# Optimization experiments

Hardware: AMD Instinct MI355X
Metric: run time of the kernel (lower is better)

The kernel has to match this reference:

```python
import jax, jax.numpy as jnp
import numpy as np

N0, N1, N2 = 360448, 22528, 2048
E0, E1 = 337920, 20480
D = 256


def setup_inputs() -> dict:
    key = jax.random.key(0)
    ks = jax.random.split(key, 12)
    s = 1.0 / np.sqrt(D)
    return {
        "x": jax.random.normal(ks[0], (N0, D), dtype=jnp.float32),
        "src0": jax.random.randint(ks[1], (E0,), 0, N0, dtype=jnp.int32),
        "dst0": jax.random.randint(ks[2], (E0,), 0, N1, dtype=jnp.int32),
        "src1": jax.random.randint(ks[3], (E1,), 0, N1, dtype=jnp.int32),
        "dst1": jax.random.randint(ks[4], (E1,), 0, N2, dtype=jnp.int32),
        "Wl0": jax.random.normal(ks[5], (D, D), dtype=jnp.float32) * s,
        "bl0": jnp.zeros((D,), dtype=jnp.float32),
        "Wr0": jax.random.normal(ks[6], (D, D), dtype=jnp.float32) * s,
        "Wl1": jax.random.normal(ks[7], (D, D), dtype=jnp.float32) * s,
        "bl1": jnp.zeros((D,), dtype=jnp.float32),
        "Wr1": jax.random.normal(ks[8], (D, D), dtype=jnp.float32) * s,
    }


def _sage_conv(x_src, x_tgt, src, dst, n_tgt, Wl, bl, Wr):
    # mean aggregation of source neighbor features per target node
    summed = jax.ops.segment_sum(x_src[src], dst, num_segments=n_tgt)
    cnt = jax.ops.segment_sum(jnp.ones((src.shape[0],), x_src.dtype), dst,
                              num_segments=n_tgt)
    agg = summed / jnp.maximum(cnt, 1.0)[:, None]
    # PyG SAGEConv: lin_l(agg) + lin_r(x_target); lin_r has no bias
    return agg @ Wl.T + bl + x_tgt @ Wr.T


def reference(x, src0, dst0, src1, dst1, Wl0, bl0, Wr0, Wl1, bl1, Wr1):
    # layer 0: [N0, D] -> [N1, D]
    h = _sage_conv(x, x[:N1], src0, dst0, N1, Wl0, bl0, Wr0)
    h = jax.nn.relu(h)  # dropout is identity in eval mode
    # layer 1: [N1, D] -> [N2, D]
    out = _sage_conv(h, h[:N2], src1, dst1, N2, Wl1, bl1, Wr1)
    return out
```

## Files before the change

kernel.cpp:

```cpp
#include <hip/hip_runtime.h>
#include <hip/hip_bf16.h>

#define N0C 360448
#define N1C 22528
#define N2C 2048

typedef __attribute__((ext_vector_type(8))) short bf16x8;
typedef __attribute__((ext_vector_type(4))) float f32x4;
typedef __attribute__((ext_vector_type(2))) int i32x2;

__device__ __forceinline__ short f2bf(float f) {
    union { float f; unsigned u; } x; x.f = f;
    unsigned r = x.u + 0x7fff + ((x.u >> 16) & 1);
    return (short)(r >> 16);
}
__device__ __forceinline__ float bf2f(unsigned short u) {
    union { unsigned u; float f; } x; x.u = ((unsigned)u) << 16;
    return x.f;
}

__global__ __launch_bounds__(256)
void prep_kernel(const float* __restrict__ Wl0, const float* __restrict__ Wr0,
                 const float* __restrict__ Wl1, const float* __restrict__ Wr1,
                 short* __restrict__ Wcat0, short* __restrict__ Wcat1,
                 int* __restrict__ hist0, int* __restrict__ hist1) {
    const int stride = gridDim.x * blockDim.x;
    const int t0 = blockIdx.x * blockDim.x + threadIdx.x;
    for (int i = t0; i < 2 * 256 * 512; i += stride) {
        int layer = i >> 17;
        int r = i & ((1 << 17) - 1);
        int j = r >> 9, k = r & 511;
        const float* Wl = layer ? Wl1 : Wl0;
        const float* Wr = layer ? Wr1 : Wr0;
        float v = (k < 256) ? Wl[j * 256 + k] : Wr[j * 256 + (k - 256)];
        (layer ? Wcat1 : Wcat0)[r] = f2bf(v);
    }
    for (int i = t0; i < N1C + N2C; i += stride) {
        if (i < N1C) hist0[i] = 0; else hist1[i - N1C] = 0;
    }
}

__global__ void hist_both_kernel(const int* __restrict__ dst0, int E0,
                                 const int* __restrict__ dst1, int E1,
                                 int* __restrict__ hist0, int* __restrict__ hist1) {
    const int stride = gridDim.x * blockDim.x;
    for (int i = blockIdx.x * blockDim.x + threadIdx.x; i < E0 + E1; i += stride) {
        if (i < E0) atomicAdd(&hist0[dst0[i]], 1);
        else        atomicAdd(&hist1[dst1[i - E0]], 1);
    }
}

__global__ __launch_bounds__(1024)
void scan_both_kernel(const int* __restrict__ hist0, int* __restrict__ rowptr0,
                      int* __restrict__ cursor0,
                      const int* __restrict__ hist1, int* __restrict__ rowptr1,
                      int* __restrict__ cursor1) {
    __shared__ int wsum[16];
    const int N = (blockIdx.x == 0) ? N1C : N2C;
    const int* hist   = (blockIdx.x == 0) ? hist0 : hist1;
    int* rowptr       = (blockIdx.x == 0) ? rowptr0 : rowptr1;
    int* cursor       = (blockIdx.x == 0) ? cursor0 : cursor1;
    const int tid = threadIdx.x;
    const int lane = tid & 63;
    const int wid = tid >> 6;
    const int per = (N + 1023) >> 10;
    const int start = min(tid * per, N);
    const int end = min(start + per, N);
    int s = 0;
    for (int i = start; i < end; ++i) s += hist[i];
    int incl = s;
#pragma unroll
    for (int d = 1; d < 64; d <<= 1) {
        int t = __shfl_up(incl, d);
        if (lane >= d) incl += t;
    }
    if (lane == 63) wsum[wid] = incl;
    __syncthreads();
    if (wid == 0) {
        int v = (lane < 16) ? wsum[lane] : 0;
#pragma unroll
        for (int d = 1; d < 16; d <<= 1) {
            int t = __shfl_up(v, d);
            if (lane >= d) v += t;
        }
        if (lane < 16) wsum[lane] = v;
    }
    __syncthreads();
    int off = (wid > 0 ? wsum[wid - 1] : 0) + (incl - s);
    for (int i = start; i < end; ++i) {
        rowptr[i] = off;
        cursor[i] = off;
        off += hist[i];
    }
    if (tid == 1023) rowptr[N] = wsum[15];
}

__global__ void fill_both_kernel(const int* __restrict__ src0, const int* __restrict__ dst0, int E0,
                                 const int* __restrict__ src1, const int* __restrict__ dst1, int E1,
                                 int* __restrict__ cursor0, int* __restrict__ eidx0,
                                 int* __restrict__ cursor1, int* __restrict__ eidx1) {
    const int stride = gridDim.x * blockDim.x;
    for (int i = blockIdx.x * blockDim.x + threadIdx.x; i < E0 + E1; i += stride) {
        if (i < E0) {
            int p = atomicAdd(&cursor0[dst0[i]], 1);
            eidx0[p] = src0[i];
        } else {
            int p = atomicAdd(&cursor1[dst1[i - E0]], 1);
            eidx1[p] = src1[i - E0];
        }
    }
}

__global__ __launch_bounds__(256)
void gather0_kernel(const float* __restrict__ x, const int* __restrict__ rowptr,
                    const int* __restrict__ eidx, short* __restrict__ Acat0) {
    const int wv = (blockIdx.x * 256 + threadIdx.x) >> 6;
    const int lane = threadIdx.x & 63;
    if (wv >= N1C) return;
    const int co = lane * 4;

    const float4 xr = *(const float4*)(x + (size_t)wv * 256 + co);

    const int beg = rowptr[wv];
    const int end = rowptr[wv + 1];
    f32x4 acc = {0.f, 0.f, 0.f, 0.f};
    f32x4 acc2 = {0.f, 0.f, 0.f, 0.f};
    int j = beg;
    for (; j + 7 < end; j += 8) {
        const f32x4 v0 = *(const f32x4*)(x + (size_t)eidx[j    ] * 256 + co);
        const f32x4 v1 = *(const f32x4*)(x + (size_t)eidx[j + 1] * 256 + co);
        const f32x4 v2 = *(const f32x4*)(x + (size_t)eidx[j + 2] * 256 + co);
        const f32x4 v3 = *(const f32x4*)(x + (size_t)eidx[j + 3] * 256 + co);
        const f32x4 v4 = *(const f32x4*)(x + (size_t)eidx[j + 4] * 256 + co);
        const f32x4 v5 = *(const f32x4*)(x + (size_t)eidx[j + 5] * 256 + co);
        const f32x4 v6 = *(const f32x4*)(x + (size_t)eidx[j + 6] * 256 + co);
        const f32x4 v7 = *(const f32x4*)(x + (size_t)eidx[j + 7] * 256 + co);
        acc  += v0 + v1 + v2 + v3;
        acc2 += v4 + v5 + v6 + v7;
    }
    for (; j + 1 < end; j += 2) {
        const f32x4 v0 = *(const f32x4*)(x + (size_t)eidx[j    ] * 256 + co);
        const f32x4 v1 = *(const f32x4*)(x + (size_t)eidx[j + 1] * 256 + co);
        acc += v0 + v1;
    }
    if (j < end)
        acc2 += *(const f32x4*)(x + (size_t)eidx[j] * 256 + co);
    acc += acc2;

    const float sc = 1.0f / fmaxf((float)(end - beg), 1.0f);
    union { short s[4]; i32x2 i; } o;
    o.s[0] = f2bf(acc.x * sc); o.s[1] = f2bf(acc.y * sc);
    o.s[2] = f2bf(acc.z * sc); o.s[3] = f2bf(acc.w * sc);
    __builtin_nontemporal_store(o.i, (i32x2*)(Acat0 + (size_t)wv * 512 + co));

    union { short s[4]; i32x2 i; } xo;
    xo.s[0] = f2bf(xr.x); xo.s[1] = f2bf(xr.y);
    xo.s[2] = f2bf(xr.z); xo.s[3] = f2bf(xr.w);
    __builtin_nontemporal_store(xo.i, (i32x2*)(Acat0 + (size_t)wv * 512 + 256 + co));
}

__global__ __launch_bounds__(256)
void gather1_kernel(const ushort* __restrict__ X, const int* __restrict__ rowptr,
                    const int* __restrict__ eidx, short* __restrict__ Acat, int N) {
    const int wv = (blockIdx.x * 256 + threadIdx.x) >> 6;
    const int lane = threadIdx.x & 63;
    if (wv >= N) return;
    const int beg = rowptr[wv];
    const int end = rowptr[wv + 1];
    float a0 = 0.f, a1 = 0.f, a2 = 0.f, a3 = 0.f;
    int j = beg;
    for (; j + 1 < end; j += 2) {
        int s0 = eidx[j], s1 = eidx[j + 1];
        ushort4 v0 = *(const ushort4*)(X + (size_t)s0 * 256 + lane * 4);
        ushort4 v1 = *(const ushort4*)(X + (size_t)s1 * 256 + lane * 4);
        a0 += bf2f(v0.x) + bf2f(v1.x); a1 += bf2f(v0.y) + bf2f(v1.y);
        a2 += bf2f(v0.z) + bf2f(v1.z); a3 += bf2f(v0.w) + bf2f(v1.w);
    }
    if (j < end) {
        ushort4 v0 = *(const ushort4*)(X + (size_t)eidx[j] * 256 + lane * 4);
        a0 += bf2f(v0.x); a1 += bf2f(v0.y); a2 += bf2f(v0.z); a3 += bf2f(v0.w);
    }
    const float sc = 1.0f / fmaxf((float)(end - beg), 1.0f);
    short4 o;
    o.x = f2bf(a0 * sc); o.y = f2bf(a1 * sc);
    o.z = f2bf(a2 * sc); o.w = f2bf(a3 * sc);
    *(short4*)(Acat + (size_t)wv * 512 + lane * 4) = o;
}

template <int CT, bool RELU, bool OUT_BF16>
__global__ __launch_bounds__(256)
void mfma_gemm_kernel(const short* __restrict__ A, const short* __restrict__ W,
                      const float* __restrict__ bias, void* __restrict__ out,
                      short* __restrict__ out2, int M) {
    const int tid = threadIdx.x;
    const int wave = tid >> 6;
    const int lane = tid & 63;
    const int r0 = blockIdx.x * 64 + wave * 16;
    const int j0 = blockIdx.y * (CT * 16);
    const int lrow = lane & 15;
    const int lk = (lane >> 4) * 8;

    const short* arow = A + (size_t)(r0 + lrow) * 512 + lk;
    const short* wbase = W + (size_t)(j0 + lrow) * 512 + lk;

    f32x4 acc[CT] = {};
#pragma unroll
    for (int ks = 0; ks < 16; ++ks) {
        bf16x8 a = *(const bf16x8*)(arow + ks * 32);
#pragma unroll
        for (int c = 0; c < CT; ++c) {
            bf16x8 b = *(const bf16x8*)(wbase + (size_t)c * 16 * 512 + ks * 32);
            acc[c] = __builtin_amdgcn_mfma_f32_16x16x32_bf16(a, b, acc[c], 0, 0, 0);
        }
    }

    const int orow = (lane >> 4) * 4;
#pragma unroll
    for (int c = 0; c < CT; ++c) {
        const int col = j0 + c * 16 + lrow;
        const float bv = bias[col];
#pragma unroll
        for (int i = 0; i < 4; ++i) {
            const int row = r0 + orow + i;
            float v = acc[c][i] + bv;
            if (RELU) v = fmaxf(v, 0.0f);
            if (OUT_BF16) {
                short hv = f2bf(v);
                ((short*)out)[(size_t)row * 256 + col] = hv;
                if (out2 != nullptr && row < N2C)
                    out2[(size_t)row * 512 + 256 + col] = hv;
            } else {
                ((float*)out)[(size_t)row * 256 + col] = v;
            }
        }
    }
}

extern "C" void kernel_launch(void* const* d_in, const int* in_sizes, int n_in,
                              void* d_out, int out_size, void* d_ws, size_t ws_size,
                              hipStream_t stream) {
    const float* x    = (const float*)d_in[0];
    const int*   src0 = (const int*)d_in[1];
    const int*   dst0 = (const int*)d_in[2];
    const int*   src1 = (const int*)d_in[3];
    const int*   dst1 = (const int*)d_in[4];
    const float* Wl0  = (const float*)d_in[5];
    const float* bl0  = (const float*)d_in[6];
    const float* Wr0  = (const float*)d_in[7];
    const float* Wl1  = (const float*)d_in[8];
    const float* bl1  = (const float*)d_in[9];
    const float* Wr1  = (const float*)d_in[10];

    const int E0 = in_sizes[1];
    const int E1 = in_sizes[3];

    char* p = (char*)d_ws;
    short* Acat0 = (short*)p;            p += (size_t)N1C * 512 * 2;
    short* h     = (short*)p;            p += (size_t)N1C * 256 * 2;
    short* Acat1 = (short*)p;            p += (size_t)N2C * 512 * 2;
    short* Wcat0 = (short*)p;            p += 256 * 512 * 2;
    short* Wcat1 = (short*)p;            p += 256 * 512 * 2;
    int* hist0   = (int*)p;              p += (size_t)N1C * 4;
    int* cursor0 = (int*)p;              p += (size_t)N1C * 4;
    int* rowptr0 = (int*)p;              p += (size_t)(N1C + 4) * 4;
    int* hist1   = (int*)p;              p += (size_t)N2C * 4;
    int* cursor1 = (int*)p;              p += (size_t)N2C * 4;
    int* rowptr1 = (int*)p;              p += (size_t)(N2C + 4) * 4;
    int* eidx0   = (int*)p;              p += (size_t)E0 * 4;
    int* eidx1   = (int*)p;              p += (size_t)E1 * 4;

    prep_kernel<<<512, 256, 0, stream>>>(Wl0, Wr0, Wl1, Wr1, Wcat0, Wcat1, hist0, hist1);
    hist_both_kernel<<<512, 256, 0, stream>>>(dst0, E0, dst1, E1, hist0, hist1);
    scan_both_kernel<<<2, 1024, 0, stream>>>(hist0, rowptr0, cursor0, hist1, rowptr1, cursor1);
    fill_both_kernel<<<512, 256, 0, stream>>>(src0, dst0, E0, src1, dst1, E1,
                                              cursor0, eidx0, cursor1, eidx1);
    gather0_kernel<<<(N1C * 64 + 255) / 256, 256, 0, stream>>>(x, rowptr0, eidx0, Acat0);
    mfma_gemm_kernel<8, true, true><<<dim3(N1C / 64, 2), 256, 0, stream>>>(
        Acat0, Wcat0, bl0, h, Acat1, N1C);
    gather1_kernel<<<(N2C * 64 + 255) / 256, 256, 0, stream>>>(
        (const ushort*)h, rowptr1, eidx1, Acat1, N2C);
    mfma_gemm_kernel<2, false, false><<<dim3(N2C / 64, 8), 256, 0, stream>>>(
        Acat1, Wcat1, bl1, (float*)d_out, nullptr, N2C);
}
```

Before: 210.9 us.

## Fuse CSR build into one cooperative kernel and use dynamic node scheduling in gather0

```diff
diff --git a/kernel.cpp b/kernel.cpp
--- a/kernel.cpp
+++ b/kernel.cpp
@@ -1,5 +1,8 @@
 #include <hip/hip_runtime.h>
 #include <hip/hip_bf16.h>
+#include <hip/hip_cooperative_groups.h>
+
+namespace cg = cooperative_groups;
 
 #define N0C 360448
 #define N1C 22528
@@ -20,12 +23,20 @@
 }
 
 __global__ __launch_bounds__(256)
-void prep_kernel(const float* __restrict__ Wl0, const float* __restrict__ Wr0,
-                 const float* __restrict__ Wl1, const float* __restrict__ Wr1,
-                 short* __restrict__ Wcat0, short* __restrict__ Wcat1,
-                 int* __restrict__ hist0, int* __restrict__ hist1) {
+void csr_coop_kernel(const float* __restrict__ Wl0, const float* __restrict__ Wr0,
+                     const float* __restrict__ Wl1, const float* __restrict__ Wr1,
+                     short* __restrict__ Wcat0, short* __restrict__ Wcat1,
+                     const int* __restrict__ src0, const int* __restrict__ dst0, int E0,
+                     const int* __restrict__ src1, const int* __restrict__ dst1, int E1,
+                     int* __restrict__ hist0, int* __restrict__ rowptr0,
+                     int* __restrict__ cursor0, int* __restrict__ eidx0,
+                     int* __restrict__ hist1, int* __restrict__ rowptr1,
+                     int* __restrict__ cursor1, int* __restrict__ eidx1,
+                     int* __restrict__ ticket) {
+    cg::grid_group grid = cg::this_grid();
     const int stride = gridDim.x * blockDim.x;
     const int t0 = blockIdx.x * blockDim.x + threadIdx.x;
+
     for (int i = t0; i < 2 * 256 * 512; i += stride) {
         int layer = i >> 17;
         int r = i & ((1 << 17) - 1);
@@ -38,69 +49,50 @@
     for (int i = t0; i < N1C + N2C; i += stride) {
         if (i < N1C) hist0[i] = 0; else hist1[i - N1C] = 0;
     }
-}
-
-__global__ void hist_both_kernel(const int* __restrict__ dst0, int E0,
-                                 const int* __restrict__ dst1, int E1,
-                                 int* __restrict__ hist0, int* __restrict__ hist1) {
-    const int stride = gridDim.x * blockDim.x;
-    for (int i = blockIdx.x * blockDim.x + threadIdx.x; i < E0 + E1; i += stride) {
+    if (t0 == 0) *ticket = 0;
+    grid.sync();
+
+    for (int i = t0; i < E0 + E1; i += stride) {
         if (i < E0) atomicAdd(&hist0[dst0[i]], 1);
         else        atomicAdd(&hist1[dst1[i - E0]], 1);
     }
-}
-
-__global__ __launch_bounds__(1024)
-void scan_both_kernel(const int* __restrict__ hist0, int* __restrict__ rowptr0,
-                      int* __restrict__ cursor0,
-                      const int* __restrict__ hist1, int* __restrict__ rowptr1,
-                      int* __restrict__ cursor1) {
-    __shared__ int wsum[16];
-    const int N = (blockIdx.x == 0) ? N1C : N2C;
-    const int* hist   = (blockIdx.x == 0) ? hist0 : hist1;
-    int* rowptr       = (blockIdx.x == 0) ? rowptr0 : rowptr1;
-    int* cursor       = (blockIdx.x == 0) ? cursor0 : cursor1;
-    const int tid = threadIdx.x;
-    const int lane = tid & 63;
-    const int wid = tid >> 6;
-    const int per = (N + 1023) >> 10;
-    const int start = min(tid * per, N);
-    const int end = min(start + per, N);
-    int s = 0;
-    for (int i = start; i < end; ++i) s += hist[i];
-    int incl = s;
-#pragma unroll
-    for (int d = 1; d < 64; d <<= 1) {
-        int t = __shfl_up(incl, d);
-        if (lane >= d) incl += t;
-    }
-    if (lane == 63) wsum[wid] = incl;
-    __syncthreads();
-    if (wid == 0) {
-        int v = (lane < 16) ? wsum[lane] : 0;
-#pragma unroll
-        for (int d = 1; d < 16; d <<= 1) {
-            int t = __shfl_up(v, d);
-            if (lane >= d) v += t;
-        }
-        if (lane < 16) wsum[lane] = v;
-    }
-    __syncthreads();
-    int off = (wid > 0 ? wsum[wid - 1] : 0) + (incl - s);
-    for (int i = start; i < end; ++i) {
-        rowptr[i] = off;
-        cursor[i] = off;
-        off += hist[i];
-    }
-    if (tid == 1023) rowptr[N] = wsum[15];
-}
-
-__global__ void fill_both_kernel(const int* __restrict__ src0, const int* __restrict__ dst0, int E0,
-                                 const int* __restrict__ src1, const int* __restrict__ dst1, int E1,
-                                 int* __restrict__ cursor0, int* __restrict__ eidx0,
-                                 int* __restrict__ cursor1, int* __restrict__ eidx1) {
-    const int stride = gridDim.x * blockDim.x;
-    for (int i = blockIdx.x * blockDim.x + threadIdx.x; i < E0 + E1; i += stride) {
+    grid.sync();
+
+    if (blockIdx.x < 2) {
+        __shared__ int wsum[4];
+        const int N = (blockIdx.x == 0) ? N1C : N2C;
+        const int* hist = (blockIdx.x == 0) ? hist0 : hist1;
+        int* rowptr     = (blockIdx.x == 0) ? rowptr0 : rowptr1;
+        int* cursor     = (blockIdx.x == 0) ? cursor0 : cursor1;
+        const int tid = threadIdx.x;
+        const int lane = tid & 63;
+        const int wid = tid >> 6;
+        const int per = (N + 255) >> 8;
+        const int start = min(tid * per, N);
+        const int end = min(start + per, N);
+        int s = 0;
+        for (int i = start; i < end; ++i) s += hist[i];
+        int incl = s;
+#pragma unroll
+        for (int d = 1; d < 64; d <<= 1) {
+            int t = __shfl_up(incl, d);
+            if (lane >= d) incl += t;
+        }
+        if (lane == 63) wsum[wid] = incl;
+        __syncthreads();
+        int woff = 0;
+        for (int k = 0; k < wid; ++k) woff += wsum[k];
+        int off = woff + (incl - s);
+        for (int i = start; i < end; ++i) {
+            rowptr[i] = off;
+            cursor[i] = off;
+            off += hist[i];
+        }
+        if (tid == 255) rowptr[N] = woff + incl;
+    }
+    grid.sync();
+
+    for (int i = t0; i < E0 + E1; i += stride) {
         if (i < E0) {
             int p = atomicAdd(&cursor0[dst0[i]], 1);
             eidx0[p] = src0[i];
@@ -113,50 +105,55 @@
 
 __global__ __launch_bounds__(256)
 void gather0_kernel(const float* __restrict__ x, const int* __restrict__ rowptr,
-                    const int* __restrict__ eidx, short* __restrict__ Acat0) {
-    const int wv = (blockIdx.x * 256 + threadIdx.x) >> 6;
+                    const int* __restrict__ eidx, short* __restrict__ Acat0,
+                    int* __restrict__ ticket) {
     const int lane = threadIdx.x & 63;
-    if (wv >= N1C) return;
     const int co = lane * 4;
-
-    const float4 xr = *(const float4*)(x + (size_t)wv * 256 + co);
-
-    const int beg = rowptr[wv];
-    const int end = rowptr[wv + 1];
-    f32x4 acc = {0.f, 0.f, 0.f, 0.f};
-    f32x4 acc2 = {0.f, 0.f, 0.f, 0.f};
-    int j = beg;
-    for (; j + 7 < end; j += 8) {
-        const f32x4 v0 = *(const f32x4*)(x + (size_t)eidx[j    ] * 256 + co);
-        const f32x4 v1 = *(const f32x4*)(x + (size_t)eidx[j + 1] * 256 + co);
-        const f32x4 v2 = *(const f32x4*)(x + (size_t)eidx[j + 2] * 256 + co);
-        const f32x4 v3 = *(const f32x4*)(x + (size_t)eidx[j + 3] * 256 + co);
-        const f32x4 v4 = *(const f32x4*)(x + (size_t)eidx[j + 4] * 256 + co);
-        const f32x4 v5 = *(const f32x4*)(x + (size_t)eidx[j + 5] * 256 + co);
-        const f32x4 v6 = *(const f32x4*)(x + (size_t)eidx[j + 6] * 256 + co);
-        const f32x4 v7 = *(const f32x4*)(x + (size_t)eidx[j + 7] * 256 + co);
-        acc  += v0 + v1 + v2 + v3;
-        acc2 += v4 + v5 + v6 + v7;
-    }
-    for (; j + 1 < end; j += 2) {
-        const f32x4 v0 = *(const f32x4*)(x + (size_t)eidx[j    ] * 256 + co);
-        const f32x4 v1 = *(const f32x4*)(x + (size_t)eidx[j + 1] * 256 + co);
-        acc += v0 + v1;
-    }
-    if (j < end)
-        acc2 += *(const f32x4*)(x + (size_t)eidx[j] * 256 + co);
-    acc += acc2;
-
-    const float sc = 1.0f / fmaxf((float)(end - beg), 1.0f);
-    union { short s[4]; i32x2 i; } o;
-    o.s[0] = f2bf(acc.x * sc); o.s[1] = f2bf(acc.y * sc);
-    o.s[2] = f2bf(acc.z * sc); o.s[3] = f2bf(acc.w * sc);
-    __builtin_nontemporal_store(o.i, (i32x2*)(Acat0 + (size_t)wv * 512 + co));
-
-    union { short s[4]; i32x2 i; } xo;
-    xo.s[0] = f2bf(xr.x); xo.s[1] = f2bf(xr.y);
-    xo.s[2] = f2bf(xr.z); xo.s[3] = f2bf(xr.w);
-    __builtin_nontemporal_store(xo.i, (i32x2*)(Acat0 + (size_t)wv * 512 + 256 + co));
+    for (;;) {
+        int node;
+        if (lane == 0) node = atomicAdd(ticket, 1);
+        node = __shfl(node, 0);
+        if (node >= N1C) return;
+
+        const float4 xr = *(const float4*)(x + (size_t)node * 256 + co);
+
+        const int beg = rowptr[node];
+        const int end = rowptr[node + 1];
+        f32x4 acc = {0.f, 0.f, 0.f, 0.f};
+        f32x4 acc2 = {0.f, 0.f, 0.f, 0.f};
+        int j = beg;
+        for (; j + 7 < end; j += 8) {
+            const f32x4 v0 = *(const f32x4*)(x + (size_t)eidx[j    ] * 256 + co);
+            const f32x4 v1 = *(const f32x4*)(x + (size_t)eidx[j + 1] * 256 + co);
+            const f32x4 v2 = *(const f32x4*)(x + (size_t)eidx[j + 2] * 256 + co);
+            const f32x4 v3 = *(const f32x4*)(x + (size_t)eidx[j + 3] * 256 + co);
+            const f32x4 v4 = *(const f32x4*)(x + (size_t)eidx[j + 4] * 256 + co);
+            const f32x4 v5 = *(const f32x4*)(x + (size_t)eidx[j + 5] * 256 + co);
+            const f32x4 v6 = *(const f32x4*)(x + (size_t)eidx[j + 6] * 256 + co);
+            const f32x4 v7 = *(const f32x4*)(x + (size_t)eidx[j + 7] * 256 + co);
+            acc  += v0 + v1 + v2 + v3;
+            acc2 += v4 + v5 + v6 + v7;
+        }
+        for (; j + 1 < end; j += 2) {
+            const f32x4 v0 = *(const f32x4*)(x + (size_t)eidx[j    ] * 256 + co);
+            const f32x4 v1 = *(const f32x4*)(x + (size_t)eidx[j + 1] * 256 + co);
+            acc += v0 + v1;
+        }
+        if (j < end)
+            acc2 += *(const f32x4*)(x + (size_t)eidx[j] * 256 + co);
+        acc += acc2;
+
+        const float sc = 1.0f / fmaxf((float)(end - beg), 1.0f);
+        union { short s[4]; i32x2 i; } o;
+        o.s[0] = f2bf(acc.x * sc); o.s[1] = f2bf(acc.y * sc);
+        o.s[2] = f2bf(acc.z * sc); o.s[3] = f2bf(acc.w * sc);
+        __builtin_nontemporal_store(o.i, (i32x2*)(Acat0 + (size_t)node * 512 + co));
+
+        union { short s[4]; i32x2 i; } xo;
+        xo.s[0] = f2bf(xr.x); xo.s[1] = f2bf(xr.y);
+        xo.s[2] = f2bf(xr.z); xo.s[3] = f2bf(xr.w);
+        __builtin_nontemporal_store(xo.i, (i32x2*)(Acat0 + (size_t)node * 512 + 256 + co));
+    }
 }
 
 __global__ __launch_bounds__(256)
@@ -251,8 +248,8 @@
     const float* bl1  = (const float*)d_in[9];
     const float* Wr1  = (const float*)d_in[10];
 
-    const int E0 = in_sizes[1];
-    const int E1 = in_sizes[3];
+    int E0 = in_sizes[1];
+    int E1 = in_sizes[3];
 
     char* p = (char*)d_ws;
     short* Acat0 = (short*)p;            p += (size_t)N1C * 512 * 2;
@@ -268,13 +265,19 @@
     int* rowptr1 = (int*)p;              p += (size_t)(N2C + 4) * 4;
     int* eidx0   = (int*)p;              p += (size_t)E0 * 4;
     int* eidx1   = (int*)p;              p += (size_t)E1 * 4;
-
-    prep_kernel<<<512, 256, 0, stream>>>(Wl0, Wr0, Wl1, Wr1, Wcat0, Wcat1, hist0, hist1);
-    hist_both_kernel<<<512, 256, 0, stream>>>(dst0, E0, dst1, E1, hist0, hist1);
-    scan_both_kernel<<<2, 1024, 0, stream>>>(hist0, rowptr0, cursor0, hist1, rowptr1, cursor1);
-    fill_both_kernel<<<512, 256, 0, stream>>>(src0, dst0, E0, src1, dst1, E1,
-                                              cursor0, eidx0, cursor1, eidx1);
-    gather0_kernel<<<(N1C * 64 + 255) / 256, 256, 0, stream>>>(x, rowptr0, eidx0, Acat0);
+    int* ticket  = (int*)p;              p += 16;
+
+    void* cargs[] = {(void*)&Wl0, (void*)&Wr0, (void*)&Wl1, (void*)&Wr1,
+                     (void*)&Wcat0, (void*)&Wcat1,
+                     (void*)&src0, (void*)&dst0, (void*)&E0,
+                     (void*)&src1, (void*)&dst1, (void*)&E1,
+                     (void*)&hist0, (void*)&rowptr0, (void*)&cursor0, (void*)&eidx0,
+                     (void*)&hist1, (void*)&rowptr1, (void*)&cursor1, (void*)&eidx1,
+                     (void*)&ticket};
+    hipLaunchCooperativeKernel(reinterpret_cast<void*>(csr_coop_kernel),
+                               dim3(512), dim3(256), cargs, 0, stream);
+
+    gather0_kernel<<<2048, 256, 0, stream>>>(x, rowptr0, eidx0, Acat0, ticket);
     mfma_gemm_kernel<8, true, true><<<dim3(N1C / 64, 2), 256, 0, stream>>>(
         Acat0, Wcat0, bl0, h, Acat1, N1C);
     gather1_kernel<<<(N2C * 64 + 255) / 256, 256, 0, stream>>>(
```

After: 701.0 us. 3.32x slower.
